# Kernel tuning notes

Measured on AMD Instinct MI355X. Metric: run time of the kernel, lower is better.

Reference implementation:

```python
import jax, jax.numpy as jnp
import numpy as np


def setup_inputs() -> dict:
    key = jax.random.key(0)
    k1, k2, k3, k4, k5 = jax.random.split(key, 5)
    B, S, H, F, E = 2, 512, 1024, 3584, 8
    scale_in = 1.0 / np.sqrt(H)
    scale_ff = 1.0 / np.sqrt(F)
    return {
        "hidden_states": jax.random.normal(k1, (B, S, H), dtype=jnp.float32),
        "gate_w": jax.random.normal(k2, (E, H), dtype=jnp.float32) * scale_in,
        "w1": jax.random.normal(k3, (E, F, H), dtype=jnp.float32) * scale_in,
        "w2": jax.random.normal(k4, (E, H, F), dtype=jnp.float32) * scale_ff,
        "w3": jax.random.normal(k5, (E, F, H), dtype=jnp.float32) * scale_in,
    }


TOP_K = 2


def reference(hidden_states, gate_w, w1, w2, w3):
    B, S, H = hidden_states.shape
    E = gate_w.shape[0]
    x = hidden_states.reshape(B * S, H)  # [T, H]
    T = x.shape[0]

    # Router: softmax in fp32, top-2 selection, renormalize selected weights.
    router_logits = x @ gate_w.T  # [T, E]
    probs = jax.nn.softmax(router_logits.astype(jnp.float32), axis=-1)
    top_vals, top_idx = jax.lax.top_k(probs, TOP_K)  # [T, K]
    top_vals = top_vals / jnp.sum(top_vals, axis=-1, keepdims=True)
    top_vals = top_vals.astype(x.dtype)

    # Dense routing-weight matrix [T, E]: weight if selected else 0
    # (equivalent to the one-hot expert_mask + index_add combine).
    dense_w = jnp.zeros((T, E), dtype=x.dtype).at[
        jnp.arange(T)[:, None], top_idx
    ].add(top_vals)

    # Expert SwiGLU MLPs, batched over the expert axis.
    h1 = jnp.einsum("th,efh->etf", x, w1)  # [E, T, F]
    h3 = jnp.einsum("th,efh->etf", x, w3)  # [E, T, F]
    y = jnp.einsum("etf,ehf->eth", jax.nn.silu(h1) * h3, w2)  # [E, T, H]

    # Weighted combine across experts.
    out = jnp.einsum("eth,te->th", y, dense_w)  # [T, H]
    return out.reshape(B, S, H), router_logits
```

## Files before the change

kernel.cpp:

```cpp
#include <hip/hip_runtime.h>
#include <hip/hip_bf16.h>

typedef __bf16 v8bf __attribute__((ext_vector_type(8)));
typedef __bf16 v4bf __attribute__((ext_vector_type(4)));
typedef float  f32x4 __attribute__((ext_vector_type(4)));
typedef unsigned int u32;

#define NTOK 1024
#define HDIM 1024
#define FDIM 3584
#define NEXP 8
#define NPAIR 2048
#define MAXT1 32
#define MAXT2 48

#define OFF_COUNTS   0
#define OFF_OFFSETS  64
#define OFF_NT1      128
#define OFF_NT2      132
#define OFF_T1E      192
#define OFF_T1M      320
#define OFF_T2E      448
#define OFF_T2M      640
#define OFF_TOKIDX   2048
#define OFF_TOKWT    (2048 + 4*NPAIR)
#define OFF_PAIRTOK  (OFF_TOKWT + 4*NPAIR)
#define OFF_PAIRWT   (OFF_PAIRTOK + 4*NPAIR)
#define OFF_SLOTOF   (OFF_PAIRWT + 4*NPAIR)
#define OFF_XB       65536
#define OFF_ACT      (OFF_XB + 2ull*NTOK*HDIM)
#define OFF_Y        (OFF_ACT + 2ull*NPAIR*FDIM)

static __device__ inline v4bf cvt4(float4 f) {
    v4bf r;
    r[0] = (__bf16)f.x; r[1] = (__bf16)f.y; r[2] = (__bf16)f.z; r[3] = (__bf16)f.w;
    return r;
}

static __device__ inline v8bf pack8(f32x4 lo, f32x4 hi) {
    v8bf r;
    r[0] = (__bf16)lo[0]; r[1] = (__bf16)lo[1]; r[2] = (__bf16)lo[2]; r[3] = (__bf16)lo[3];
    r[4] = (__bf16)hi[0]; r[5] = (__bf16)hi[1]; r[6] = (__bf16)hi[2]; r[7] = (__bf16)hi[3];
    return r;
}

#define FENCE() asm volatile("" ::: "memory")
#define BARRIER() do { FENCE(); __builtin_amdgcn_s_barrier(); FENCE(); } while (0)
#define WAITVM(N) asm volatile("s_waitcnt vmcnt(" #N ")" ::: "memory")

#define DMA16(SRC, DST) \
    __builtin_amdgcn_global_load_lds((const __attribute__((address_space(1))) u32*)(SRC), \
                                     (__attribute__((address_space(3))) u32*)(DST), 16, 0, 0)

__global__ __launch_bounds__(256) void moe_cvtx(const float* __restrict__ x,
                                                __bf16* __restrict__ xb)
{
    const size_t i = ((size_t)blockIdx.x * 256 + threadIdx.x) * 4;
    float4 v = *(const float4*)(x + i);
    *(v4bf*)(xb + i) = cvt4(v);
}

__global__ __launch_bounds__(256) void moe_router(
    const float* __restrict__ x, const float* __restrict__ gw,
    float* __restrict__ logits, int* __restrict__ counts,
    int* __restrict__ tok_idx, float* __restrict__ tok_wt)
{
    const int lane = threadIdx.x & 63;
    const int wv = threadIdx.x >> 6;
    const int t = blockIdx.x * 4 + wv;
    const float* xr = x + (size_t)t * HDIM;

    float acc[NEXP];
#pragma unroll
    for (int e = 0; e < NEXP; ++e) acc[e] = 0.f;
#pragma unroll
    for (int j = 0; j < 4; ++j) {
        int h = lane * 4 + j * 256;
        float4 xv = *(const float4*)(xr + h);
#pragma unroll
        for (int e = 0; e < NEXP; ++e) {
            float4 g = *(const float4*)(gw + e * HDIM + h);
            acc[e] += xv.x * g.x + xv.y * g.y + xv.z * g.z + xv.w * g.w;
        }
    }
#pragma unroll
    for (int e = 0; e < NEXP; ++e) {
#pragma unroll
        for (int s = 32; s > 0; s >>= 1) acc[e] += __shfl_xor(acc[e], s);
    }
    if (lane == 0) {
#pragma unroll
        for (int e = 0; e < NEXP; ++e) logits[t * NEXP + e] = acc[e];
        int i0 = 0;
#pragma unroll
        for (int e = 1; e < NEXP; ++e) if (acc[e] > acc[i0]) i0 = e;
        int i1 = (i0 == 0) ? 1 : 0;
#pragma unroll
        for (int e = 0; e < NEXP; ++e) if (e != i0 && acc[e] > acc[i1]) i1 = e;
        float w0 = 1.f / (1.f + expf(acc[i1] - acc[i0]));
        float w1 = 1.f - w0;
        tok_idx[2 * t] = i0; tok_idx[2 * t + 1] = i1;
        tok_wt[2 * t] = w0;  tok_wt[2 * t + 1] = w1;
        atomicAdd(&counts[i0], 1);
        atomicAdd(&counts[i1], 1);
    }
}

__global__ void moe_scatter(const int* __restrict__ counts, const int* __restrict__ tok_idx,
                            const float* __restrict__ tok_wt, int* __restrict__ offsets,
                            int* __restrict__ pair_token, float* __restrict__ pair_wt,
                            int* __restrict__ slot_of,
                            int* __restrict__ t1e, int* __restrict__ t1m, int* __restrict__ nt1,
                            int* __restrict__ t2e, int* __restrict__ t2m, int* __restrict__ nt2)
{
    __shared__ int cur[NEXP];
    const int tid = threadIdx.x;
    if (tid == 0) {
        int run = 0, n1 = 0, n2 = 0;
        for (int e = 0; e < NEXP; ++e) {
            offsets[e] = run; cur[e] = run;
            for (int m0 = 0; m0 < counts[e]; m0 += 128) { t1e[n1] = e; t1m[n1] = m0; ++n1; }
            for (int m0 = 0; m0 < counts[e]; m0 += 64)  { t2e[n2] = e; t2m[n2] = m0; ++n2; }
            run += counts[e];
        }
        *nt1 = n1; *nt2 = n2;
    }
    __syncthreads();
    for (int p = tid; p < 2 * NTOK; p += blockDim.x) {
        int e = tok_idx[p];
        int s = atomicAdd(&cur[e], 1);
        pair_token[s] = p >> 1;
        pair_wt[s] = tok_wt[p];
        slot_of[p] = s;
    }
}

__global__ __launch_bounds__(256, 2) void moe_gemm1(
    const __bf16* __restrict__ xb, const float* __restrict__ w1g,
    const float* __restrict__ w3g, const int* __restrict__ counts,
    const int* __restrict__ offsets, const int* __restrict__ pair_token,
    const int* __restrict__ t1e, const int* __restrict__ t1m,
    const int* __restrict__ nt1,
    __bf16* __restrict__ act)
{
    const int ty = blockIdx.y;
    if (ty >= *nt1) return;
    const int e = t1e[ty];
    const int m0 = t1m[ty];
    const int Me = counts[e];
    const int rows = min(128, Me - m0);
    const int slot0 = offsets[e] + m0;
    const int n0 = blockIdx.x * 64;

    __shared__ __align__(16) __bf16 As[2][128 * 32];
    __shared__ __align__(16) float  B1s[2][64 * 32];
    __shared__ __align__(16) float  B3s[2][64 * 32];

    const int tid = threadIdx.x;
    const int lane = tid & 63;
    const int wv = tid >> 6;
    const int wm = (wv >> 1) * 64;
    const int wn = (wv & 1) * 32;
    const int lr = lane & 15;
    const int lk = (lane >> 4) * 8;

    f32x4 acc1[4][2], acc3[4][2];
#pragma unroll
    for (int i = 0; i < 4; ++i)
#pragma unroll
        for (int j = 0; j < 2; ++j) {
            acc1[i][j] = (f32x4){0.f, 0.f, 0.f, 0.f};
            acc3[i][j] = (f32x4){0.f, 0.f, 0.f, 0.f};
        }

    const char* asrc[2];
#pragma unroll
    for (int i = 0; i < 2; ++i) {
        int c = i * 256 + tid;
        int r = c >> 2;
        int rr = (r < rows) ? r : 0;
        int sj = (c & 3) ^ (r & 3);
        asrc[i] = (const char*)(xb + (size_t)pair_token[slot0 + rr] * HDIM + sj * 8);
    }
    const int adst_base0 = (0 * 256 + wv * 64) * 16;
    const int adst_base1 = (1 * 256 + wv * 64) * 16;

    const char* b1src[2];
#pragma unroll
    for (int i = 0; i < 2; ++i) {
        int c = i * 256 + tid;
        int r = c >> 3;
        int sj = (c & 7) ^ (r & 7);
        b1src[i] = (const char*)(w1g + ((size_t)e * FDIM + n0 + r) * HDIM + sj * 4);
    }
    const ptrdiff_t d31b = (const char*)w3g - (const char*)w1g;
    const int bdst_base0 = (0 * 256 + wv * 64) * 16;
    const int bdst_base1 = (1 * 256 + wv * 64) * 16;

    int aoff[4], boff[2];
#pragma unroll
    for (int i = 0; i < 4; ++i) {
        int row = wm + i * 16 + lr;
        aoff[i] = (row * 64 + lk * 2) ^ ((row & 3) << 4);
    }
#pragma unroll
    for (int i = 0; i < 2; ++i) {
        int row = wn + i * 16 + lr;
        boff[i] = (row * 128 + lk * 4) ^ ((row & 7) << 4);
    }

#define DMA_ALL1(BUF, K0) do { \
    DMA16(asrc[0] + (size_t)(K0) * 2, (char*)&As[BUF][0] + adst_base0); \
    DMA16(asrc[1] + (size_t)(K0) * 2, (char*)&As[BUF][0] + adst_base1); \
    DMA16(b1src[0] + (size_t)(K0) * 4, (char*)&B1s[BUF][0] + bdst_base0); \
    DMA16(b1src[1] + (size_t)(K0) * 4, (char*)&B1s[BUF][0] + bdst_base1); \
    DMA16(b1src[0] + d31b + (size_t)(K0) * 4, (char*)&B3s[BUF][0] + bdst_base0); \
    DMA16(b1src[1] + d31b + (size_t)(K0) * 4, (char*)&B3s[BUF][0] + bdst_base1); \
} while (0)

#define CMP1(BUF) do { \
    v8bf af[4], b1f[2], b3f[2]; \
    _Pragma("unroll") \
    for (int i = 0; i < 4; ++i) af[i] = *(const v8bf*)((const char*)&As[BUF][0] + aoff[i]); \
    _Pragma("unroll") \
    for (int i = 0; i < 2; ++i) { \
        f32x4 lo1 = *(const f32x4*)((const char*)&B1s[BUF][0] + boff[i]); \
        f32x4 hi1 = *(const f32x4*)((const char*)&B1s[BUF][0] + (boff[i] ^ 16)); \
        f32x4 lo3 = *(const f32x4*)((const char*)&B3s[BUF][0] + boff[i]); \
        f32x4 hi3 = *(const f32x4*)((const char*)&B3s[BUF][0] + (boff[i] ^ 16)); \
        b1f[i] = pack8(lo1, hi1); \
        b3f[i] = pack8(lo3, hi3); \
    } \
    _Pragma("unroll") \
    for (int mi = 0; mi < 4; ++mi) { \
        _Pragma("unroll") \
        for (int ni = 0; ni < 2; ++ni) { \
            acc1[mi][ni] = __builtin_amdgcn_mfma_f32_16x16x32_bf16(af[mi], b1f[ni], acc1[mi][ni], 0, 0, 0); \
            acc3[mi][ni] = __builtin_amdgcn_mfma_f32_16x16x32_bf16(af[mi], b3f[ni], acc3[mi][ni], 0, 0, 0); \
        } } } while (0)

    DMA_ALL1(0, 0);
    int buf = 0;
    for (int ks = 0; ks < HDIM / 32; ++ks) {
        if (ks + 1 < HDIM / 32) {
            DMA_ALL1(buf ^ 1, (ks + 1) * 32);
            WAITVM(6);
        } else {
            WAITVM(0);
        }
        BARRIER();
        CMP1(buf);
        BARRIER();
        buf ^= 1;
    }
#undef DMA_ALL1
#undef CMP1

    const int rj = (lane >> 4) * 4;
#pragma unroll
    for (int mi = 0; mi < 4; ++mi) {
#pragma unroll
        for (int j = 0; j < 4; ++j) {
            int rm = wm + mi * 16 + rj + j;
            if (rm < rows) {
                size_t rowoff = (size_t)(slot0 + rm) * FDIM + n0 + wn;
#pragma unroll
                for (int ni = 0; ni < 2; ++ni) {
                    float h1 = acc1[mi][ni][j];
                    float h3 = acc3[mi][ni][j];
                    float sv = (h1 / (1.f + __expf(-h1))) * h3;
                    act[rowoff + ni * 16 + lr] = (__bf16)sv;
                }
            }
        }
    }
}

__global__ __launch_bounds__(256, 2) void moe_gemm2(
    const __bf16* __restrict__ act, const float* __restrict__ w2g,
    const int* __restrict__ counts, const int* __restrict__ offsets,
    const int* __restrict__ t2e, const int* __restrict__ t2m,
    const int* __restrict__ nt2,
    float* __restrict__ y)
{
    const int ty = blockIdx.y;
    if (ty >= *nt2) return;
    const int e = t2e[ty];
    const int m0 = t2m[ty];
    const int Me = counts[e];
    const int rows = min(64, Me - m0);
    const int slot0 = offsets[e] + m0;
    const int n0 = blockIdx.x * 32;

    __shared__ __align__(16) __bf16 As[2][64 * 32];
    __shared__ __align__(16) float  Bs[2][32 * 32];

    const int tid = threadIdx.x;
    const int lane = tid & 63;
    const int wv = tid >> 6;
    const int wm = (wv >> 1) * 32;
    const int wn = (wv & 1) * 16;
    const int lr = lane & 15;
    const int lk = (lane >> 4) * 8;

    f32x4 acc[2];
    acc[0] = (f32x4){0.f, 0.f, 0.f, 0.f};
    acc[1] = (f32x4){0.f, 0.f, 0.f, 0.f};

    const char* asrc;
    {
        int c = tid;
        int r = c >> 2;
        int rr = (r < rows) ? r : 0;
        int sj = (c & 3) ^ (r & 3);
        asrc = (const char*)(act + (size_t)(slot0 + rr) * FDIM + sj * 8);
    }
    const int adst_base = (wv * 64) * 16;
    const char* bsrc;
    {
        int c = tid;
        int r = c >> 3;
        int sj = (c & 7) ^ (r & 7);
        bsrc = (const char*)(w2g + ((size_t)e * HDIM + n0 + r) * FDIM + sj * 4);
    }
    const int bdst_base = (wv * 64) * 16;

    int aoff[2], boff;
#pragma unroll
    for (int i = 0; i < 2; ++i) {
        int row = wm + i * 16 + lr;
        aoff[i] = (row * 64 + lk * 2) ^ ((row & 3) << 4);
    }
    {
        int row = wn + lr;
        boff = (row * 128 + lk * 4) ^ ((row & 7) << 4);
    }

#define DMA_ALL2(BUF, K0) do { \
    DMA16(asrc + (size_t)(K0) * 2, (char*)&As[BUF][0] + adst_base); \
    DMA16(bsrc + (size_t)(K0) * 4, (char*)&Bs[BUF][0] + bdst_base); \
} while (0)

#define CMP2(BUF) do { \
    v8bf af[2], bf; \
    _Pragma("unroll") \
    for (int i = 0; i < 2; ++i) af[i] = *(const v8bf*)((const char*)&As[BUF][0] + aoff[i]); \
    { \
        f32x4 lo = *(const f32x4*)((const char*)&Bs[BUF][0] + boff); \
        f32x4 hi = *(const f32x4*)((const char*)&Bs[BUF][0] + (boff ^ 16)); \
        bf = pack8(lo, hi); \
    } \
    acc[0] = __builtin_amdgcn_mfma_f32_16x16x32_bf16(af[0], bf, acc[0], 0, 0, 0); \
    acc[1] = __builtin_amdgcn_mfma_f32_16x16x32_bf16(af[1], bf, acc[1], 0, 0, 0); \
} while (0)

    DMA_ALL2(0, 0);
    int buf = 0;
    for (int ks = 0; ks < FDIM / 32; ++ks) {
        if (ks + 1 < FDIM / 32) {
            DMA_ALL2(buf ^ 1, (ks + 1) * 32);
            WAITVM(2);
        } else {
            WAITVM(0);
        }
        BARRIER();
        CMP2(buf);
        BARRIER();
        buf ^= 1;
    }
#undef DMA_ALL2
#undef CMP2

    const int rj = (lane >> 4) * 4;
#pragma unroll
    for (int mi = 0; mi < 2; ++mi) {
#pragma unroll
        for (int j = 0; j < 4; ++j) {
            int rm = wm + mi * 16 + rj + j;
            if (rm < rows) {
                y[(size_t)(slot0 + rm) * HDIM + n0 + wn + lr] = acc[mi][j];
            }
        }
    }
}

__global__ __launch_bounds__(256) void moe_combine(
    const float* __restrict__ y, const int* __restrict__ slot_of,
    const float* __restrict__ pair_wt, float* __restrict__ out)
{
    const int t = blockIdx.x;
    const int tid = threadIdx.x;
    const int s0 = slot_of[2 * t];
    const int s1 = slot_of[2 * t + 1];
    const float w0 = pair_wt[s0];
    const float w1 = pair_wt[s1];
    const float4 a = *(const float4*)(y + (size_t)s0 * HDIM + tid * 4);
    const float4 b = *(const float4*)(y + (size_t)s1 * HDIM + tid * 4);
    float4 o;
    o.x = w0 * a.x + w1 * b.x;
    o.y = w0 * a.y + w1 * b.y;
    o.z = w0 * a.z + w1 * b.z;
    o.w = w0 * a.w + w1 * b.w;
    *(float4*)(out + (size_t)t * HDIM + tid * 4) = o;
}

extern "C" void kernel_launch(void* const* d_in, const int* in_sizes, int n_in,
                              void* d_out, int out_size, void* d_ws, size_t ws_size,
                              hipStream_t stream) {
    const float* x   = (const float*)d_in[0];
    const float* gw  = (const float*)d_in[1];
    const float* w1  = (const float*)d_in[2];
    const float* w2  = (const float*)d_in[3];
    const float* w3  = (const float*)d_in[4];

    float* out    = (float*)d_out;
    float* logits = out + (size_t)NTOK * HDIM;

    char* ws = (char*)d_ws;
    int*    counts     = (int*)(ws + OFF_COUNTS);
    int*    offsets    = (int*)(ws + OFF_OFFSETS);
    int*    nt1        = (int*)(ws + OFF_NT1);
    int*    nt2        = (int*)(ws + OFF_NT2);
    int*    t1e        = (int*)(ws + OFF_T1E);
    int*    t1m        = (int*)(ws + OFF_T1M);
    int*    t2e        = (int*)(ws + OFF_T2E);
    int*    t2m        = (int*)(ws + OFF_T2M);
    int*    tok_idx    = (int*)(ws + OFF_TOKIDX);
    float*  tok_wt     = (float*)(ws + OFF_TOKWT);
    int*    pair_token = (int*)(ws + OFF_PAIRTOK);
    float*  pair_wt    = (float*)(ws + OFF_PAIRWT);
    int*    slot_of    = (int*)(ws + OFF_SLOTOF);
    __bf16* xb         = (__bf16*)(ws + OFF_XB);
    __bf16* act        = (__bf16*)(ws + OFF_ACT);
    float*  yb         = (float*)(ws + OFF_Y);

    hipMemsetAsync(counts, 0, 64, stream);

    moe_cvtx<<<dim3(NTOK * HDIM / 1024), dim3(256), 0, stream>>>(x, xb);
    moe_router<<<dim3(NTOK / 4), dim3(256), 0, stream>>>(x, gw, logits, counts, tok_idx, tok_wt);
    moe_scatter<<<dim3(1), dim3(256), 0, stream>>>(counts, tok_idx, tok_wt, offsets,
                                                   pair_token, pair_wt, slot_of,
                                                   t1e, t1m, nt1, t2e, t2m, nt2);
    moe_gemm1<<<dim3(FDIM / 64, MAXT1), dim3(256), 0, stream>>>(
        xb, w1, w3, counts, offsets, pair_token, t1e, t1m, nt1, act);
    moe_gemm2<<<dim3(HDIM / 32, MAXT2), dim3(256), 0, stream>>>(
        act, w2, counts, offsets, t2e, t2m, nt2, yb);
    moe_combine<<<dim3(NTOK), dim3(256), 0, stream>>>(yb, slot_of, pair_wt, out);
}
```

Before: 229.1 us.

## Widen K tile to 64, single-buffer loads, split-K gemm2 into two partials

Both grouped GEMMs now stage a 64-wide K slice per iteration with 16-way swizzled LDS layouts. This replaces the 32-wide double-buffered pipeline with single-buffered load-wait-compute steps, halving barrier count per K but exposing global load latency. gemm2 also widens its N tile to 64 and splits K in two across blockIdx.z, writing two partial outputs that the combine kernel sums. The split raises gemm2 parallelism at the cost of an extra fp32 y buffer of traffic.

```diff
diff --git a/kernel.cpp b/kernel.cpp
--- a/kernel.cpp
+++ b/kernel.cpp
@@ -13,6 +13,8 @@
 #define NPAIR 2048
 #define MAXT1 32
 #define MAXT2 48
+#define KSPLIT2 2
+#define KPER2 (FDIM / KSPLIT2)
 
 #define OFF_COUNTS   0
 #define OFF_OFFSETS  64
@@ -29,7 +31,8 @@
 #define OFF_SLOTOF   (OFF_PAIRWT + 4*NPAIR)
 #define OFF_XB       65536
 #define OFF_ACT      (OFF_XB + 2ull*NTOK*HDIM)
-#define OFF_Y        (OFF_ACT + 2ull*NPAIR*FDIM)
+#define OFF_Y0       (OFF_ACT + 2ull*NPAIR*FDIM)
+#define OFF_Y1       (OFF_Y0 + 4ull*NPAIR*HDIM)
 
 static __device__ inline v4bf cvt4(float4 f) {
     v4bf r;
@@ -46,7 +49,8 @@
 
 #define FENCE() asm volatile("" ::: "memory")
 #define BARRIER() do { FENCE(); __builtin_amdgcn_s_barrier(); FENCE(); } while (0)
-#define WAITVM(N) asm volatile("s_waitcnt vmcnt(" #N ")" ::: "memory")
+#define WAITVM0() asm volatile("s_waitcnt vmcnt(0)" ::: "memory")
+#define WAITLGKM0() asm volatile("s_waitcnt lgkmcnt(0)" ::: "memory")
 
 #define DMA16(SRC, DST) \
     __builtin_amdgcn_global_load_lds((const __attribute__((address_space(1))) u32*)(SRC), \
@@ -152,17 +156,17 @@
     const int slot0 = offsets[e] + m0;
     const int n0 = blockIdx.x * 64;
 
-    __shared__ __align__(16) __bf16 As[2][128 * 32];
-    __shared__ __align__(16) float  B1s[2][64 * 32];
-    __shared__ __align__(16) float  B3s[2][64 * 32];
+    __shared__ __align__(16) __bf16 As[128 * 64];
+    __shared__ __align__(16) float  B1s[64 * 64];
+    __shared__ __align__(16) float  B3s[64 * 64];
 
     const int tid = threadIdx.x;
     const int lane = tid & 63;
     const int wv = tid >> 6;
+    const int ln4 = lane >> 4;
+    const int lr = lane & 15;
     const int wm = (wv >> 1) * 64;
     const int wn = (wv & 1) * 32;
-    const int lr = lane & 15;
-    const int lk = (lane >> 4) * 8;
 
     f32x4 acc1[4][2], acc3[4][2];
 #pragma unroll
@@ -173,90 +177,84 @@
             acc3[i][j] = (f32x4){0.f, 0.f, 0.f, 0.f};
         }
 
-    const char* asrc[2];
-#pragma unroll
-    for (int i = 0; i < 2; ++i) {
-        int c = i * 256 + tid;
-        int r = c >> 2;
-        int rr = (r < rows) ? r : 0;
-        int sj = (c & 3) ^ (r & 3);
-        asrc[i] = (const char*)(xb + (size_t)pair_token[slot0 + rr] * HDIM + sj * 8);
-    }
-    const int adst_base0 = (0 * 256 + wv * 64) * 16;
-    const int adst_base1 = (1 * 256 + wv * 64) * 16;
-
-    const char* b1src[2];
-#pragma unroll
-    for (int i = 0; i < 2; ++i) {
+    const char* asrc[4];
+#pragma unroll
+    for (int i = 0; i < 4; ++i) {
         int c = i * 256 + tid;
         int r = c >> 3;
+        int rr = (r < rows) ? r : 0;
         int sj = (c & 7) ^ (r & 7);
-        b1src[i] = (const char*)(w1g + ((size_t)e * FDIM + n0 + r) * HDIM + sj * 4);
+        asrc[i] = (const char*)(xb + (size_t)pair_token[slot0 + rr] * HDIM) + sj * 16;
+    }
+    const char* bsrc[4];
+#pragma unroll
+    for (int i = 0; i < 4; ++i) {
+        int c = i * 256 + tid;
+        int r = c >> 4;
+        int sj = (c & 15) ^ (r & 15);
+        bsrc[i] = (const char*)(w1g + ((size_t)e * FDIM + n0 + r) * HDIM) + sj * 16;
     }
     const ptrdiff_t d31b = (const char*)w3g - (const char*)w1g;
-    const int bdst_base0 = (0 * 256 + wv * 64) * 16;
-    const int bdst_base1 = (1 * 256 + wv * 64) * 16;
-
-    int aoff[4], boff[2];
+
+#define DMA_ALL1(K0) do { _Pragma("unroll") \
+    for (int i = 0; i < 4; ++i) { \
+        DMA16(asrc[i] + (size_t)(K0) * 128, (char*)As + (i * 256 + wv * 64) * 16); \
+        DMA16(bsrc[i] + (size_t)(K0) * 256, (char*)B1s + (i * 256 + wv * 64) * 16); \
+        DMA16(bsrc[i] + d31b + (size_t)(K0) * 256, (char*)B3s + (i * 256 + wv * 64) * 16); \
+    } } while (0)
+
+    int abase[4], axor[4];
 #pragma unroll
     for (int i = 0; i < 4; ++i) {
         int row = wm + i * 16 + lr;
-        aoff[i] = (row * 64 + lk * 2) ^ ((row & 3) << 4);
-    }
+        abase[i] = row * 128;
+        axor[i] = (row & 7) << 4;
+    }
+    int bbase[2], bxor[2];
 #pragma unroll
     for (int i = 0; i < 2; ++i) {
         int row = wn + i * 16 + lr;
-        boff[i] = (row * 128 + lk * 4) ^ ((row & 7) << 4);
-    }
-
-#define DMA_ALL1(BUF, K0) do { \
-    DMA16(asrc[0] + (size_t)(K0) * 2, (char*)&As[BUF][0] + adst_base0); \
-    DMA16(asrc[1] + (size_t)(K0) * 2, (char*)&As[BUF][0] + adst_base1); \
-    DMA16(b1src[0] + (size_t)(K0) * 4, (char*)&B1s[BUF][0] + bdst_base0); \
-    DMA16(b1src[1] + (size_t)(K0) * 4, (char*)&B1s[BUF][0] + bdst_base1); \
-    DMA16(b1src[0] + d31b + (size_t)(K0) * 4, (char*)&B3s[BUF][0] + bdst_base0); \
-    DMA16(b1src[1] + d31b + (size_t)(K0) * 4, (char*)&B3s[BUF][0] + bdst_base1); \
-} while (0)
-
-#define CMP1(BUF) do { \
-    v8bf af[4], b1f[2], b3f[2]; \
-    _Pragma("unroll") \
-    for (int i = 0; i < 4; ++i) af[i] = *(const v8bf*)((const char*)&As[BUF][0] + aoff[i]); \
-    _Pragma("unroll") \
-    for (int i = 0; i < 2; ++i) { \
-        f32x4 lo1 = *(const f32x4*)((const char*)&B1s[BUF][0] + boff[i]); \
-        f32x4 hi1 = *(const f32x4*)((const char*)&B1s[BUF][0] + (boff[i] ^ 16)); \
-        f32x4 lo3 = *(const f32x4*)((const char*)&B3s[BUF][0] + boff[i]); \
-        f32x4 hi3 = *(const f32x4*)((const char*)&B3s[BUF][0] + (boff[i] ^ 16)); \
-        b1f[i] = pack8(lo1, hi1); \
-        b3f[i] = pack8(lo3, hi3); \
-    } \
-    _Pragma("unroll") \
-    for (int mi = 0; mi < 4; ++mi) { \
-        _Pragma("unroll") \
-        for (int ni = 0; ni < 2; ++ni) { \
-            acc1[mi][ni] = __builtin_amdgcn_mfma_f32_16x16x32_bf16(af[mi], b1f[ni], acc1[mi][ni], 0, 0, 0); \
-            acc3[mi][ni] = __builtin_amdgcn_mfma_f32_16x16x32_bf16(af[mi], b3f[ni], acc3[mi][ni], 0, 0, 0); \
-        } } } while (0)
-
-    DMA_ALL1(0, 0);
-    int buf = 0;
-    for (int ks = 0; ks < HDIM / 32; ++ks) {
-        if (ks + 1 < HDIM / 32) {
-            DMA_ALL1(buf ^ 1, (ks + 1) * 32);
-            WAITVM(6);
-        } else {
-            WAITVM(0);
-        }
+        bbase[i] = row * 256;
+        bxor[i] = (row & 15) << 4;
+    }
+
+#define CMP1() do { \
+    v8bf af[4][2]; v8bf b1f[2][2], b3f[2][2]; \
+    _Pragma("unroll") \
+    for (int mi = 0; mi < 4; ++mi) { _Pragma("unroll") \
+        for (int ks = 0; ks < 2; ++ks) \
+            af[mi][ks] = *(const v8bf*)((const char*)As + abase[mi] + ((ks * 64 + ln4 * 16) ^ axor[mi])); } \
+    _Pragma("unroll") \
+    for (int ni = 0; ni < 2; ++ni) { _Pragma("unroll") \
+        for (int ks = 0; ks < 2; ++ks) { \
+            int in0 = ks * 128 + ln4 * 32; \
+            f32x4 lo1 = *(const f32x4*)((const char*)B1s + bbase[ni] + ((in0) ^ bxor[ni])); \
+            f32x4 hi1 = *(const f32x4*)((const char*)B1s + bbase[ni] + ((in0 + 16) ^ bxor[ni])); \
+            f32x4 lo3 = *(const f32x4*)((const char*)B3s + bbase[ni] + ((in0) ^ bxor[ni])); \
+            f32x4 hi3 = *(const f32x4*)((const char*)B3s + bbase[ni] + ((in0 + 16) ^ bxor[ni])); \
+            b1f[ni][ks] = pack8(lo1, hi1); \
+            b3f[ni][ks] = pack8(lo3, hi3); } } \
+    _Pragma("unroll") \
+    for (int mi = 0; mi < 4; ++mi) { _Pragma("unroll") \
+        for (int ni = 0; ni < 2; ++ni) { _Pragma("unroll") \
+            for (int ks = 0; ks < 2; ++ks) { \
+                acc1[mi][ni] = __builtin_amdgcn_mfma_f32_16x16x32_bf16(af[mi][ks], b1f[ni][ks], acc1[mi][ni], 0, 0, 0); \
+                acc3[mi][ni] = __builtin_amdgcn_mfma_f32_16x16x32_bf16(af[mi][ks], b3f[ni][ks], acc3[mi][ni], 0, 0, 0); } } } \
+    } while (0)
+
+    DMA_ALL1(0);
+    for (int ks = 0; ks < HDIM / 64; ++ks) {
+        WAITVM0();
         BARRIER();
-        CMP1(buf);
+        CMP1();
+        WAITLGKM0();
         BARRIER();
-        buf ^= 1;
+        if (ks + 1 < HDIM / 64) DMA_ALL1(ks + 1);
     }
 #undef DMA_ALL1
 #undef CMP1
 
-    const int rj = (lane >> 4) * 4;
+    const int rj = ln4 * 4;
 #pragma unroll
     for (int mi = 0; mi < 4; ++mi) {
 #pragma unroll
@@ -281,7 +279,7 @@
     const int* __restrict__ counts, const int* __restrict__ offsets,
     const int* __restrict__ t2e, const int* __restrict__ t2m,
     const int* __restrict__ nt2,
-    float* __restrict__ y)
+    float* __restrict__ y0, float* __restrict__ y1)
 {
     const int ty = blockIdx.y;
     if (ty >= *nt2) return;
@@ -290,103 +288,122 @@
     const int Me = counts[e];
     const int rows = min(64, Me - m0);
     const int slot0 = offsets[e] + m0;
-    const int n0 = blockIdx.x * 32;
-
-    __shared__ __align__(16) __bf16 As[2][64 * 32];
-    __shared__ __align__(16) float  Bs[2][32 * 32];
+    const int n0 = blockIdx.x * 64;
+    const int kz = blockIdx.z;
+    float* yout = kz ? y1 : y0;
+    const size_t kbase = (size_t)kz * KPER2;
+
+    __shared__ __align__(16) __bf16 As[64 * 64];
+    __shared__ __align__(16) float  Bs[64 * 64];
 
     const int tid = threadIdx.x;
     const int lane = tid & 63;
     const int wv = tid >> 6;
+    const int ln4 = lane >> 4;
+    const int lr = lane & 15;
     const int wm = (wv >> 1) * 32;
-    const int wn = (wv & 1) * 16;
-    const int lr = lane & 15;
-    const int lk = (lane >> 4) * 8;
-
-    f32x4 acc[2];
-    acc[0] = (f32x4){0.f, 0.f, 0.f, 0.f};
-    acc[1] = (f32x4){0.f, 0.f, 0.f, 0.f};
-
-    const char* asrc;
-    {
-        int c = tid;
-        int r = c >> 2;
+    const int wn = (wv & 1) * 32;
+
+    f32x4 acc[2][2];
+#pragma unroll
+    for (int i = 0; i < 2; ++i)
+#pragma unroll
+        for (int j = 0; j < 2; ++j) acc[i][j] = (f32x4){0.f, 0.f, 0.f, 0.f};
+
+    const char* asrc[2];
+#pragma unroll
+    for (int i = 0; i < 2; ++i) {
+        int c = i * 256 + tid;
+        int r = c >> 3;
         int rr = (r < rows) ? r : 0;
-        int sj = (c & 3) ^ (r & 3);
-        asrc = (const char*)(act + (size_t)(slot0 + rr) * FDIM + sj * 8);
-    }
-    const int adst_base = (wv * 64) * 16;
-    const char* bsrc;
-    {
-        int c = tid;
-        int r = c >> 3;
         int sj = (c & 7) ^ (r & 7);
-        bsrc = (const char*)(w2g + ((size_t)e * HDIM + n0 + r) * FDIM + sj * 4);
-    }
-    const int bdst_base = (wv * 64) * 16;
-
-    int aoff[2], boff;
+        asrc[i] = (const char*)(act + (size_t)(slot0 + rr) * FDIM + kbase) + sj * 16;
+    }
+    const char* bsrc[4];
+#pragma unroll
+    for (int i = 0; i < 4; ++i) {
+        int c = i * 256 + tid;
+        int r = c >> 4;
+        int sj = (c & 15) ^ (r & 15);
+        bsrc[i] = (const char*)(w2g + ((size_t)e * HDIM + n0 + r) * FDIM + kbase) + sj * 16;
+    }
+
+#define DMA_ALL2(K0) do { \
+    _Pragma("unroll") \
+    for (int i = 0; i < 2; ++i) \
+        DMA16(asrc[i] + (size_t)(K0) * 128, (char*)As + (i * 256 + wv * 64) * 16); \
+    _Pragma("unroll") \
+    for (int i = 0; i < 4; ++i) \
+        DMA16(bsrc[i] + (size_t)(K0) * 256, (char*)Bs + (i * 256 + wv * 64) * 16); \
+    } while (0)
+
+    int abase[2], axor[2];
 #pragma unroll
     for (int i = 0; i < 2; ++i) {
         int row = wm + i * 16 + lr;
-        aoff[i] = (row * 64 + lk * 2) ^ ((row & 3) << 4);
-    }
-    {
-        int row = wn + lr;
-        boff = (row * 128 + lk * 4) ^ ((row & 7) << 4);
-    }
-
-#define DMA_ALL2(BUF, K0) do { \
-    DMA16(asrc + (size_t)(K0) * 2, (char*)&As[BUF][0] + adst_base); \
-    DMA16(bsrc + (size_t)(K0) * 4, (char*)&Bs[BUF][0] + bdst_base); \
-} while (0)
-
-#define CMP2(BUF) do { \
-    v8bf af[2], bf; \
-    _Pragma("unroll") \
-    for (int i = 0; i < 2; ++i) af[i] = *(const v8bf*)((const char*)&As[BUF][0] + aoff[i]); \
-    { \
-        f32x4 lo = *(const f32x4*)((const char*)&Bs[BUF][0] + boff); \
-        f32x4 hi = *(const f32x4*)((const char*)&Bs[BUF][0] + (boff ^ 16)); \
-        bf = pack8(lo, hi); \
-    } \
-    acc[0] = __builtin_amdgcn_mfma_f32_16x16x32_bf16(af[0], bf, acc[0], 0, 0, 0); \
-    acc[1] = __builtin_amdgcn_mfma_f32_16x16x32_bf16(af[1], bf, acc[1], 0, 0, 0); \
-} while (0)
-
-    DMA_ALL2(0, 0);
-    int buf = 0;
-    for (int ks = 0; ks < FDIM / 32; ++ks) {
-        if (ks + 1 < FDIM / 32) {
-            DMA_ALL2(buf ^ 1, (ks + 1) * 32);
-            WAITVM(2);
-        } else {
-            WAITVM(0);
-        }
+        abase[i] = row * 128;
+        axor[i] = (row & 7) << 4;
+    }
+    int bbase[2], bxor[2];
+#pragma unroll
+    for (int i = 0; i < 2; ++i) {
+        int row = wn + i * 16 + lr;
+        bbase[i] = row * 256;
+        bxor[i] = (row & 15) << 4;
+    }
+
+#define CMP2() do { \
+    v8bf af[2][2], bf[2][2]; \
+    _Pragma("unroll") \
+    for (int mi = 0; mi < 2; ++mi) { _Pragma("unroll") \
+        for (int ks = 0; ks < 2; ++ks) \
+            af[mi][ks] = *(const v8bf*)((const char*)As + abase[mi] + ((ks * 64 + ln4 * 16) ^ axor[mi])); } \
+    _Pragma("unroll") \
+    for (int ni = 0; ni < 2; ++ni) { _Pragma("unroll") \
+        for (int ks = 0; ks < 2; ++ks) { \
+            int in0 = ks * 128 + ln4 * 32; \
+            f32x4 lo = *(const f32x4*)((const char*)Bs + bbase[ni] + ((in0) ^ bxor[ni])); \
+            f32x4 hi = *(const f32x4*)((const char*)Bs + bbase[ni] + ((in0 + 16) ^ bxor[ni])); \
+            bf[ni][ks] = pack8(lo, hi); } } \
+    _Pragma("unroll") \
+    for (int mi = 0; mi < 2; ++mi) { _Pragma("unroll") \
+        for (int ni = 0; ni < 2; ++ni) { _Pragma("unroll") \
+            for (int ks = 0; ks < 2; ++ks) \
+                acc[mi][ni] = __builtin_amdgcn_mfma_f32_16x16x32_bf16(af[mi][ks], bf[ni][ks], acc[mi][ni], 0, 0, 0); } } \
+    } while (0)
+
+    DMA_ALL2(0);
+    for (int ks = 0; ks < KPER2 / 64; ++ks) {
+        WAITVM0();
         BARRIER();
-        CMP2(buf);
+        CMP2();
+        WAITLGKM0();
         BARRIER();
-        buf ^= 1;
+        if (ks + 1 < KPER2 / 64) DMA_ALL2(ks + 1);
     }
 #undef DMA_ALL2
 #undef CMP2
 
-    const int rj = (lane >> 4) * 4;
+    const int rj = ln4 * 4;
 #pragma unroll
     for (int mi = 0; mi < 2; ++mi) {
 #pragma unroll
         for (int j = 0; j < 4; ++j) {
             int rm = wm + mi * 16 + rj + j;
             if (rm < rows) {
-                y[(size_t)(slot0 + rm) * HDIM + n0 + wn + lr] = acc[mi][j];
+                size_t rowoff = (size_t)(slot0 + rm) * HDIM + n0 + wn;
+#pragma unroll
+                for (int ni = 0; ni < 2; ++ni)
+                    yout[rowoff + ni * 16 + lr] = acc[mi][ni][j];
             }
         }
     }
 }
 
 __global__ __launch_bounds__(256) void moe_combine(
-    const float* __restrict__ y, const int* __restrict__ slot_of,
-    const float* __restrict__ pair_wt, float* __restrict__ out)
+    const float* __restrict__ y0, const float* __restrict__ y1,
+    const int* __restrict__ slot_of, const float* __restrict__ pair_wt,
+    float* __restrict__ out)
 {
     const int t = blockIdx.x;
     const int tid = threadIdx.x;
@@ -394,13 +411,15 @@
     const int s1 = slot_of[2 * t + 1];
     const float w0 = pair_wt[s0];
     const float w1 = pair_wt[s1];
-    const float4 a = *(const float4*)(y + (size_t)s0 * HDIM + tid * 4);
-    const float4 b = *(const float4*)(y + (size_t)s1 * HDIM + tid * 4);
+    const float4 a0 = *(const float4*)(y0 + (size_t)s0 * HDIM + tid * 4);
+    const float4 a1 = *(const float4*)(y1 + (size_t)s0 * HDIM + tid * 4);
+    const float4 b0 = *(const float4*)(y0 + (size_t)s1 * HDIM + tid * 4);
+    const float4 b1 = *(const float4*)(y1 + (size_t)s1 * HDIM + tid * 4);
     float4 o;
-    o.x = w0 * a.x + w1 * b.x;
-    o.y = w0 * a.y + w1 * b.y;
-    o.z = w0 * a.z + w1 * b.z;
-    o.w = w0 * a.w + w1 * b.w;
+    o.x = w0 * (a0.x + a1.x) + w1 * (b0.x + b1.x);
+    o.y = w0 * (a0.y + a1.y) + w1 * (b0.y + b1.y);
+    o.z = w0 * (a0.z + a1.z) + w1 * (b0.z + b1.z);
+    o.w = w0 * (a0.w + a1.w) + w1 * (b0.w + b1.w);
     *(float4*)(out + (size_t)t * HDIM + tid * 4) = o;
 }
 
@@ -432,7 +451,8 @@
     int*    slot_of    = (int*)(ws + OFF_SLOTOF);
     __bf16* xb         = (__bf16*)(ws + OFF_XB);
     __bf16* act        = (__bf16*)(ws + OFF_ACT);
-    float*  yb         = (float*)(ws + OFF_Y);
+    float*  yb0        = (float*)(ws + OFF_Y0);
+    float*  yb1        = (float*)(ws + OFF_Y1);
 
     hipMemsetAsync(counts, 0, 64, stream);
 
@@ -443,7 +463,7 @@
                                                    t1e, t1m, nt1, t2e, t2m, nt2);
     moe_gemm1<<<dim3(FDIM / 64, MAXT1), dim3(256), 0, stream>>>(
         xb, w1, w3, counts, offsets, pair_token, t1e, t1m, nt1, act);
-    moe_gemm2<<<dim3(HDIM / 32, MAXT2), dim3(256), 0, stream>>>(
-        act, w2, counts, offsets, t2e, t2m, nt2, yb);
-    moe_combine<<<dim3(NTOK), dim3(256), 0, stream>>>(yb, slot_of, pair_wt, out);
-}
+    moe_gemm2<<<dim3(HDIM / 64, MAXT2, KSPLIT2), dim3(256), 0, stream>>>(
+        act, w2, counts, offsets, t2e, t2m, nt2, yb0, yb1);
+    moe_combine<<<dim3(NTOK), dim3(256), 0, stream>>>(yb0, yb1, slot_of, pair_wt, out);
+}
```

After: 196.3 us. 14.3% less time.
